# Kernel tuning notes

Hardware: AMD Instinct MI355X
Metric: run time of the kernel (lower is better)

## Reference

```python
import jax, jax.numpy as jnp
import numpy as np

B, N, D, E, F, K = 2, 2048, 768, 8, 3072, 2
V_MAX = 3.0
FEAT_CLAMP = 10.0


def setup_inputs() -> dict:
    key = jax.random.key(0)
    ks = jax.random.split(key, 8)
    s = lambda k, shape, sc: (jax.random.normal(k, shape, jnp.float32) * sc)
    return {
        "x": s(ks[0], (B, N, D), 1.0),
        "v_w": s(ks[1], (D,), 0.02),
        "v_b": jnp.zeros((), jnp.float32),
        "gate_w": s(ks[2], (D, E), 0.02),
        "gate_b": jnp.zeros((E,), jnp.float32),
        "w1": s(ks[3], (E, D, F), 0.02),
        "b1": jnp.zeros((E, F), jnp.float32),
        "w2": s(ks[4], (E, F, D), 0.02),
        "b2": jnp.zeros((E, D), jnp.float32),
        "out_w": s(ks[5], (2, D), 0.02),
        "out_b": jnp.zeros((D,), jnp.float32),
        "bk_scale": jnp.ones((D,), jnp.float32),
    }


def bk_green_diag(a):
    # a: (B, N) complex64 diagonal of (H_eps - z), unit off-diagonals.
    # Stable two-sided continued-fraction (Thomas/LDU) recursion:
    #   d_i = a_i - 1/d_{i-1},  e_i = a_i - 1/e_{i+1},  G_ii = 1/(d_i + e_i - a_i)
    aT = jnp.swapaxes(a, 0, 1)  # (N, B)

    def step(c, ai):
        d = ai - 1.0 / c
        return d, d

    d0 = aT[0]
    _, d_rest = jax.lax.scan(step, d0, aT[1:])
    d = jnp.concatenate([d0[None], d_rest], axis=0)  # (N, B)

    eN = aT[-1]
    _, e_rest = jax.lax.scan(step, eN, aT[:-1], reverse=True)
    e = jnp.concatenate([e_rest, eN[None]], axis=0)  # (N, B)

    G = 1.0 / (d + e - aT)
    return jnp.swapaxes(G, 0, 1)  # (B, N) complex


def reference(x, v_w, v_b, gate_w, gate_b, w1, b1, w2, b2, out_w, out_b, bk_scale):
    # --- potential projection: v = clamp(Linear(x), +-3) ---
    v = jnp.clip(x @ v_w + v_b, -V_MAX, V_MAX)  # (B, N)
    # H_eps diagonal = -2 + v, z = 1j  ->  A = H_eps - z
    a = ((-2.0 + v).astype(jnp.complex64) - 1j)
    G = bk_green_diag(a)  # (B, N) complex
    feats = jnp.stack([G.real, G.imag], axis=-1)  # (B, N, 2)

    # --- sparse MoE FFN (top-k softmax gating, GELU experts) ---
    logits = x @ gate_w + gate_b  # (B, N, E)
    probs = jax.nn.softmax(logits, axis=-1)
    topv, topi = jax.lax.top_k(probs, K)
    topv = topv / jnp.sum(topv, axis=-1, keepdims=True)
    comb = jnp.sum(topv[..., None] * jax.nn.one_hot(topi, E, dtype=x.dtype), axis=2)  # (B, N, E)
    h = jax.nn.gelu(jnp.einsum("bnd,edf->bnef", x, w1) + b1)  # (B, N, E, F)
    y = jnp.einsum("bnef,efd->bned", h, w2) + b2  # (B, N, E, D)
    ffn_out = jnp.einsum("bne,bned->bnd", comb, y)

    # --- spectral branch: clamp features, project to d_model, scale ---
    feats_c = jnp.clip(feats, -FEAT_CLAMP, FEAT_CLAMP)
    spec_out = feats_c @ out_w + out_b  # (B, N, D)
    return ffn_out + bk_scale * spec_out
```

## Files before the change

kernel.cpp:

```cpp
#include <hip/hip_runtime.h>
#include <hip/hip_bf16.h>

#define BB 2
#define NN 2048
#define DD 768
#define EE 8
#define FF 3072
#define TOK (BB*NN)
#define ROWS_CAP 9216
#define TILES 72

typedef __attribute__((ext_vector_type(8))) __bf16 bf16x8;
typedef __attribute__((ext_vector_type(4))) float floatx4;

#define OFF_CTRL    0ull
#define OFF_V       1024ull
#define OFF_TOKE    17408ull
#define OFF_TOKW    50176ull
#define OFF_ROWTOK  82944ull
#define OFF_ROWW    119808ull
#define OFF_SLOT    156672ull
#define OFF_FEATS   189440ull
#define OFF_W2T     222208ull
#define OFF_XBF     37970944ull
#define OFF_W1T     44262400ull
#define OFF_H       82011136ull
#define OFF_Y       OFF_XBF

__device__ __forceinline__ ushort f2b(float f) {
    union { float f; unsigned int i; } v; v.f = f;
    unsigned int u = v.i;
    unsigned int r = (u + 0x7FFFu + ((u >> 16) & 1u)) >> 16;
    return (ushort)r;
}
__device__ __forceinline__ unsigned int pk2(float lo, float hi) {
    union { float f; unsigned int u; } a, b;
    a.f = lo; b.f = hi;
    unsigned int ra = ((a.u + 0x7FFFu + ((a.u >> 16) & 1u)) >> 16) & 0xFFFFu;
    unsigned int rb = (b.u + 0x7FFFu + ((b.u >> 16) & 1u)) & 0xFFFF0000u;
    return ra | rb;
}
__device__ __forceinline__ float gelu_f(float x) {
    float z = 0.7978845608028654f * x * (1.f + 0.044715f * x * x);
    z = fminf(fmaxf(z, -12.f), 12.f);
    float e = __expf(2.f * z);
    return 0.5f * x * (1.f + (e - 1.f) / (e + 1.f));
}
__device__ __forceinline__ void gload16(const ushort* g, ushort* l) {
    __builtin_amdgcn_global_load_lds((const __attribute__((address_space(1))) void*)g,
                                     (__attribute__((address_space(3))) void*)l,
                                     16, 0, 0);
}

struct cplx { float x, y; };
__device__ __forceinline__ cplx cmulc(cplx a, cplx b) { return {a.x*b.x - a.y*b.y, a.x*b.y + a.y*b.x}; }
__device__ __forceinline__ cplx caddc(cplx a, cplx b) { return {a.x + b.x, a.y + b.y}; }
__device__ __forceinline__ cplx cdivc(cplx a, cplx b) {
    float s = 1.f / (b.x*b.x + b.y*b.y);
    return {(a.x*b.x + a.y*b.y)*s, (a.y*b.x - a.x*b.y)*s};
}
struct mob { cplx m00, m01, m10, m11; };
__device__ __forceinline__ mob mmul(const mob& A, const mob& B) {
    mob C;
    C.m00 = caddc(cmulc(A.m00, B.m00), cmulc(A.m01, B.m10));
    C.m01 = caddc(cmulc(A.m00, B.m01), cmulc(A.m01, B.m11));
    C.m10 = caddc(cmulc(A.m10, B.m00), cmulc(A.m11, B.m10));
    C.m11 = caddc(cmulc(A.m10, B.m01), cmulc(A.m11, B.m11));
    return C;
}
__device__ __forceinline__ void mnorm(mob& A) {
    float s = fabsf(A.m00.x);
    s = fmaxf(s, fabsf(A.m00.y)); s = fmaxf(s, fabsf(A.m01.x)); s = fmaxf(s, fabsf(A.m01.y));
    s = fmaxf(s, fabsf(A.m10.x)); s = fmaxf(s, fabsf(A.m10.y)); s = fmaxf(s, fabsf(A.m11.x));
    s = fmaxf(s, fabsf(A.m11.y));
    float r = 1.f / fmaxf(s, 1e-30f);
    A.m00.x *= r; A.m00.y *= r; A.m01.x *= r; A.m01.y *= r;
    A.m10.x *= r; A.m10.y *= r; A.m11.x *= r; A.m11.y *= r;
}
__device__ __forceinline__ mob mstep(cplx a, const mob& P) {
    mob C;
    C.m00 = {a.x*P.m00.x - a.y*P.m00.y - P.m10.x, a.x*P.m00.y + a.y*P.m00.x - P.m10.y};
    C.m01 = {a.x*P.m01.x - a.y*P.m01.y - P.m11.x, a.x*P.m01.y + a.y*P.m01.x - P.m11.y};
    C.m10 = P.m00; C.m11 = P.m01;
    return C;
}
__device__ __forceinline__ void mstore(float* s, const mob& A) {
    s[0]=A.m00.x; s[1]=A.m00.y; s[2]=A.m01.x; s[3]=A.m01.y;
    s[4]=A.m10.x; s[5]=A.m10.y; s[6]=A.m11.x; s[7]=A.m11.y;
}
__device__ __forceinline__ mob mload(const float* s) {
    mob A;
    A.m00 = {s[0], s[1]}; A.m01 = {s[2], s[3]};
    A.m10 = {s[4], s[5]}; A.m11 = {s[6], s[7]};
    return A;
}

template<bool PERM>
__device__ __forceinline__ void tcvt64_body(
    const float* __restrict__ src, ushort* __restrict__ dst,
    int Rs, int Cs, int r0, int c0, ushort* __restrict__ tT , int tid)
{
    int lr = tid >> 2;
    int lc0 = (tid & 3) * 16;
    const float* sp = src + (size_t)(r0 + lr) * Cs + c0 + lc0;
    float4 v[4];
    #pragma unroll
    for (int u = 0; u < 4; u++) v[u] = *(const float4*)(sp + 4*u);
    int chw = lr >> 3, wbit = lr & 7;
    #pragma unroll
    for (int u = 0; u < 4; u++) {
        float vs[4] = {v[u].x, v[u].y, v[u].z, v[u].w};
        #pragma unroll
        for (int e2 = 0; e2 < 4; e2++) {
            int col = lc0 + 4*u + e2;
            int g = (col >> 4) & 3;
            tT[col * 72 + ((chw ^ g) << 3) + wbit] = f2b(vs[e2]);
        }
    }
    __syncthreads();
    int p = tid & 7;
    #pragma unroll
    for (int pass = 0; pass < 2; pass++) {
        int c = (tid >> 3) + pass * 32;
        int g = (c >> 4) & 3;
        int chl = p ^ g;
        int a64 = chl * 8;
        size_t off = (size_t)(c0 + c) * Rs + r0 + a64;
        if (PERM) {
            int g32 = (a64 >> 5) * 32;
            int a = a64 & 31;
            ushort o8[8] __attribute__((aligned(16)));
            #pragma unroll
            for (int k = 0; k < 8; k++) {
                int pk = a + k;
                int rl = g32 + (pk >> 1) + ((pk & 1) << 4);
                int phys = ((rl >> 3) ^ g) * 8 + (rl & 7);
                o8[k] = tT[c * 72 + phys];
            }
            *(uint4*)(dst + off) = *(const uint4*)o8;
        } else {
            *(uint4*)(dst + off) = *(const uint4*)(tT + c * 72 + p * 8);
        }
    }
}

#define NB_CVT   ((TOK*DD)/8/256)
#define NB_ROUTE (TOK/4)

__device__ __forceinline__ void cvt_body(const float* __restrict__ src, ushort* __restrict__ dst, int i) {
    const float4* s = ((const float4*)src) + (size_t)i * 2;
    float4 a = s[0], b = s[1];
    uint4 o;
    o.x = pk2(a.x, a.y); o.y = pk2(a.z, a.w);
    o.z = pk2(b.x, b.y); o.w = pk2(b.z, b.w);
    *(((uint4*)dst) + i) = o;
}

__device__ __forceinline__ void routing_body(
    const float* __restrict__ x, const float* __restrict__ v_w, const float* __restrict__ v_b,
    const float* __restrict__ gate_w, const float* __restrict__ gate_b,
    float* __restrict__ v_out, int* __restrict__ tok_e, float* __restrict__ tok_w, int blk)
{
    int wave = threadIdx.x >> 6, lane = threadIdx.x & 63;
    int t = blk * 4 + wave;
    const float* xr = x + (size_t)t * DD;
    float av = 0.f;
    float ag[8] = {0.f, 0.f, 0.f, 0.f, 0.f, 0.f, 0.f, 0.f};
    #pragma unroll
    for (int i = 0; i < 12; i++) {
        int d = lane + 64 * i;
        float xv = xr[d];
        av += xv * v_w[d];
        const float4* g = (const float4*)(gate_w + d * 8);
        float4 g0 = g[0], g1 = g[1];
        ag[0] += xv * g0.x; ag[1] += xv * g0.y; ag[2] += xv * g0.z; ag[3] += xv * g0.w;
        ag[4] += xv * g1.x; ag[5] += xv * g1.y; ag[6] += xv * g1.z; ag[7] += xv * g1.w;
    }
    #pragma unroll
    for (int off = 32; off >= 1; off >>= 1) {
        av += __shfl_xor(av, off);
        #pragma unroll
        for (int e = 0; e < 8; e++) ag[e] += __shfl_xor(ag[e], off);
    }
    if (lane == 0) {
        float vv = av + v_b[0];
        vv = fminf(fmaxf(vv, -3.f), 3.f);
        v_out[t] = vv;
        float lg[8];
        #pragma unroll
        for (int e = 0; e < 8; e++) lg[e] = ag[e] + gate_b[e];
        int e0 = 0;
        #pragma unroll
        for (int e = 1; e < 8; e++) if (lg[e] > lg[e0]) e0 = e;
        int e1 = -1;
        #pragma unroll
        for (int e = 0; e < 8; e++) if (e != e0 && (e1 < 0 || lg[e] > lg[e1])) e1 = e;
        float w0 = 1.f / (1.f + __expf(lg[e1] - lg[e0]));
        tok_e[2*t] = e0; tok_e[2*t+1] = e1;
        tok_w[2*t] = w0; tok_w[2*t+1] = 1.f - w0;
    }
}

__global__ __launch_bounds__(256) void prep0_kernel(
    const float* __restrict__ x, ushort* __restrict__ x_bf,
    const float* __restrict__ v_w, const float* __restrict__ v_b,
    const float* __restrict__ gate_w, const float* __restrict__ gate_b,
    float* __restrict__ v_out, int* __restrict__ tok_e, float* __restrict__ tok_w)
{
    int id = blockIdx.x;
    if (id < NB_CVT) { cvt_body(x, x_bf, id * 256 + threadIdx.x); return; }
    id -= NB_CVT;
    routing_body(x, v_w, v_b, gate_w, gate_b, v_out, tok_e, tok_w, id);
}

#define NB_W1T4  (12*48*EE/4)

__device__ void setup_body(
    const int* __restrict__ tok_e, const float* __restrict__ tok_w,
    int* __restrict__ ctrl, int* __restrict__ row_token, float* __restrict__ row_w,
    int* __restrict__ slot)
{
    __shared__ int cnt[8], base[8], cursor[8];
    int tid = threadIdx.x;
    int lane = tid & 63;
    if (tid < 8) { cnt[tid] = 0; cursor[tid] = 0; }
    __syncthreads();

    int mye[8];
    #pragma unroll
    for (int it = 0; it < 8; it++) {
        int idx = it * 1024 + tid;
        int e = tok_e[idx];
        mye[it] = e;
        #pragma unroll
        for (int ex = 0; ex < 8; ex++) {
            unsigned long long m = __ballot(e == ex);
            if (e == ex && lane == (__ffsll((long long)m) - 1))
                atomicAdd(&cnt[ex], (int)__popcll(m));
        }
    }
    __syncthreads();
    if (tid == 0) {
        int b = 0;
        int* te = ctrl + 24;
        for (int i = 0; i < TILES; i++) te[i] = -1;
        #pragma unroll
        for (int e = 0; e < EE; e++) {
            base[e] = b;
            ctrl[16 + e] = b;
            int tiles = (cnt[e] + 127) >> 7;
            int t0 = b >> 7;
            for (int i = 0; i < tiles; i++) te[t0 + i] = e;
            b += tiles << 7;
        }
    }
    for (int p = tid; p < ROWS_CAP; p += 1024) row_token[p] = -1;
    __syncthreads();

    #pragma unroll
    for (int it = 0; it < 8; it++) {
        int idx = it * 1024 + tid;
        int e = mye[it];
        unsigned long long lt = (1ull << lane) - 1ull;
        int p = 0;
        #pragma unroll
        for (int ex = 0; ex < 8; ex++) {
            unsigned long long m = __ballot(e == ex);
            if (e == ex) {
                int leader = __ffsll((long long)m) - 1;
                int pos = (int)__popcll(m & lt);
                int bp = 0;
                if (lane == leader) bp = atomicAdd(&cursor[ex], (int)__popcll(m));
                bp = __shfl(bp, leader);
                p = base[ex] + bp + pos;
            }
        }
        row_token[p] = idx >> 1;
        row_w[p] = tok_w[idx];
        slot[idx] = p;
    }
}

__device__ void bk_body(int b, const float* __restrict__ v, float* __restrict__ feats) {
    int t = threadIdx.x;
    bool act = t < 256;
    __shared__ float sm[256][8];
    const mob I = {{1.f,0.f},{0.f,0.f},{0.f,0.f},{1.f,0.f}};
    cplx a[8];
    const float* vb = v + (size_t)b * NN;
    if (act) {
        #pragma unroll
        for (int j = 0; j < 8; j++) { a[j].x = -2.f + vb[t*8 + j]; a[j].y = -1.f; }
    }

    mob cur = I;
    if (act) {
        #pragma unroll
        for (int j = 0; j < 8; j++) cur = mstep(a[j], cur);
        mnorm(cur);
        mstore(sm[t], cur);
    }
    for (int s = 1; s < 256; s <<= 1) {
        __syncthreads();
        mob prev; bool has = act && (t >= s);
        if (has) prev = mload(sm[t - s]);
        __syncthreads();
        if (has) { cur = mmul(cur, prev); mnorm(cur); mstore(sm[t], cur); }
    }
    __syncthreads();
    cplx dreg[8];
    if (act) {
        mob P = (t > 0) ? mload(sm[t - 1]) : I;
        #pragma unroll
        for (int j = 0; j < 8; j++) {
            P = mstep(a[j], P); mnorm(P);
            dreg[j] = cdivc(P.m00, P.m10);
        }
    }
    __syncthreads();

    cur = I;
    if (act) {
        #pragma unroll
        for (int j = 7; j >= 0; j--) cur = mstep(a[j], cur);
        mnorm(cur);
        mstore(sm[t], cur);
    }
    for (int s = 1; s < 256; s <<= 1) {
        __syncthreads();
        mob nxt; bool has = act && (t + s < 256);
        if (has) nxt = mload(sm[t + s]);
        __syncthreads();
        if (has) { cur = mmul(cur, nxt); mnorm(cur); mstore(sm[t], cur); }
    }
    __syncthreads();
    if (act) {
        mob P = (t < 255) ? mload(sm[t + 1]) : I;
        #pragma unroll
        for (int j = 7; j >= 0; j--) {
            P = mstep(a[j], P); mnorm(P);
            cplx e = cdivc(P.m00, P.m10);
            cplx den = {dreg[j].x + e.x - a[j].x, dreg[j].y + e.y - a[j].y};
            cplx one = {1.f, 0.f};
            cplx G = cdivc(one, den);
            int i = b * NN + t*8 + j;
            feats[2*i]   = G.x;
            feats[2*i+1] = G.y;
        }
    }
}

__global__ __launch_bounds__(1024) void setup_bk_kernel(
    const int* __restrict__ tok_e, const float* __restrict__ tok_w,
    int* __restrict__ ctrl, int* __restrict__ row_token, float* __restrict__ row_w,
    int* __restrict__ slot, const float* __restrict__ v, float* __restrict__ feats,
    const float* __restrict__ w1, ushort* __restrict__ w1t)
{
    if (blockIdx.x == 0) { setup_body(tok_e, tok_w, ctrl, row_token, row_w, slot); return; }
    if (blockIdx.x <= BB) { bk_body(blockIdx.x - 1, v, feats); return; }
    __shared__ __align__(16) ushort tT4[4 * 4608];
    int tt = (blockIdx.x - 1 - BB) * 4 + (threadIdx.x >> 8);
    int e = tt / (12 * 48);
    int rem = tt - e * 12 * 48;
    int cy = rem / 12;
    int rx = rem - cy * 12;
    tcvt64_body<false>(w1 + (size_t)e * DD * FF, w1t + (size_t)e * FF * DD,
                       DD, FF, rx * 64, cy * 64,
                       tT4 + (threadIdx.x >> 8) * 4608, threadIdx.x & 255);
}

#define MFMAS() do { \
        _Pragma("unroll") \
        for (int i = 0; i < 4; i++) \
            _Pragma("unroll") \
            for (int j = 0; j < 4; j++) \
                acc[i][j] = __builtin_amdgcn_mfma_f32_16x16x32_bf16(afr[i], bfr[j], acc[i][j], 0, 0, 0); \
    } while (0)

#define G1N   (72 * 12)
#define NW2T  (48 * 12 * EE / 2)

__global__ __launch_bounds__(512, 2) void gemm1_fused_kernel(
    const ushort* __restrict__ x_bf, const ushort* __restrict__ w1t, const float* __restrict__ b1,
    const int* __restrict__ ctrl, const int* __restrict__ row_token, ushort* __restrict__ H,
    const float* __restrict__ w2, ushort* __restrict__ w2t)
{
    __shared__ __align__(16) ushort SH[73728];
    __shared__ int toks[128];
    int bid = blockIdx.x;
    int tid = threadIdx.x;

    if (bid >= G1N) {
        int tt = (bid - G1N) * 2 + (tid >> 8);
        int e = tt / (48 * 12);
        int rem = tt - e * 48 * 12;
        int cy = rem / 48;
        int rx = rem - cy * 48;
        ushort* tT = SH + (tid >> 8) * 4608;
        tcvt64_body<true>(w2 + (size_t)e * FF * DD, w2t + (size_t)e * DD * FF,
                          FF, DD, rx * 64, cy * 64, tT, tid & 255);
        return;
    }

    int x = bid & 7, s = bid >> 3;
    int fx = s / 9;
    int tile = x * 9 + (s - fx * 9);
    int e = ctrl[24 + tile];
    if (e < 0) return;
    int p0 = tile * 128;
    int f0 = fx * 256;

    ushort* B3 = SH + 3 * 8192;

    if (tid < 128) { int tk = row_token[p0 + tid]; toks[tid] = tk < 0 ? 0 : tk; }
    __syncthreads();

    int wave = tid >> 6, lane = tid & 63;
    int wr = wave >> 2, wc = wave & 3;
    int w16 = wave * 16;

    int srow = lane >> 3;
    int kq = ((lane & 7) ^ srow) * 8;
    int tokA0 = toks[w16 + srow];
    int tokA1 = toks[w16 + 8 + srow];
    const ushort* aA0 = x_bf + (size_t)tokA0 * DD + kq;
    const ushort* aA1 = x_bf + (size_t)tokA1 * DD + kq;
    const ushort* w1e = w1t + (size_t)e * (FF * DD);
    const ushort* bB00 = w1e + (size_t)(f0 +       w16 + srow) * DD + kq;
    const ushort* bB01 = w1e + (size_t)(f0 +       w16 + 8 + srow) * DD + kq;
    const ushort* bB10 = w1e + (size_t)(f0 + 128 + w16 + srow) * DD + kq;
    const ushort* bB11 = w1e + (size_t)(f0 + 128 + w16 + 8 + srow) * DD + kq;
    int dA0 = w16 * 64;
    int dA1 = dA0 + 512;

    int lm = lane & 15, q = lane >> 4;
    int qa0 = ((q    ) ^ (lm & 7)) * 8;
    int qa1 = ((q | 4) ^ (lm & 7)) * 8;
    int arow = (wr * 64 + lm) * 64;
    int brow = (wc * 64 + lm) * 64;

    floatx4 zero4 = {0.f, 0.f, 0.f, 0.f};
    floatx4 acc[4][4];
    #pragma unroll
    for (int i = 0; i < 4; i++)
        #pragma unroll
        for (int j = 0; j < 4; j++) acc[i][j] = zero4;

    #define STG_A(SL, kt) do { \
        gload16(aA0 + (kt)*64, SH + (SL)*8192 + dA0); \
        gload16(aA1 + (kt)*64, SH + (SL)*8192 + dA1); } while (0)
    #define STG_B(SL, kt) do { \
        gload16(bB00 + (kt)*64, B3 + (SL)*16384 + dA0); \
        gload16(bB01 + (kt)*64, B3 + (SL)*16384 + dA1); \
        gload16(bB10 + (kt)*64, B3 + (SL)*16384 + 8192 + dA0); \
        gload16(bB11 + (kt)*64, B3 + (SL)*16384 + 8192 + dA1); } while (0)

    #define G1_PHASE(SL, QH) do { \
        bf16x8 afr[4], bfr[4]; \
        _Pragma("unroll") \
        for (int i = 0; i < 4; i++) \
            afr[i] = *(const bf16x8*)(const void*)(SH + (SL)*8192 + arow + i*1024 + (QH)); \
        _Pragma("unroll") \
        for (int j = 0; j < 4; j++) \
            bfr[j] = *(const bf16x8*)(const void*)(B3 + (SL)*16384 + brow + j*1024 + (QH)); \
        asm volatile("s_waitcnt lgkmcnt(0)" ::: "memory"); \
        __builtin_amdgcn_sched_barrier(0); \
        __builtin_amdgcn_s_setprio(1); \
        MFMAS(); \
        __builtin_amdgcn_s_setprio(0); } while (0)

    #define G1_TILE(kt, SL, S2) do { \
        bool st_ = (kt) < 10; \
        if (st_) STG_A(S2, (kt) + 2); \
        G1_PHASE(SL, qa0); \
        __builtin_amdgcn_s_barrier(); \
        if (st_) STG_B(S2, (kt) + 2); \
        G1_PHASE(SL, qa1); \
        if (st_)            { asm volatile("s_waitcnt vmcnt(6)" ::: "memory"); } \
        else if ((kt) < 11) { asm volatile("s_waitcnt vmcnt(0)" ::: "memory"); } \
        __builtin_amdgcn_s_barrier(); } while (0)

    STG_A(0, 0); STG_B(0, 0);
    STG_A(1, 1); STG_B(1, 1);
    asm volatile("s_waitcnt vmcnt(6)" ::: "memory");
    __builtin_amdgcn_s_barrier();

    for (int kb = 0; kb < 12; kb += 3) {
        G1_TILE(kb    , 0, 2);
        G1_TILE(kb + 1, 1, 0);
        G1_TILE(kb + 2, 2, 1);
    }
    #undef G1_TILE
    #undef G1_PHASE
    #undef STG_B
    #undef STG_A

    #pragma unroll
    for (int i = 0; i < 4; i++) {
        #pragma unroll
        for (int jp = 0; jp < 2; jp++) {
            float bias0 = b1[e * FF + f0 + wc*64 + (2*jp)*16 + lm];
            float bias1 = b1[e * FF + f0 + wc*64 + (2*jp+1)*16 + lm];
            #pragma unroll
            for (int r = 0; r < 4; r++) {
                int m = wr*64 + i*16 + q*4 + r;
                float h0 = gelu_f(acc[i][2*jp][r] + bias0);
                float h1 = gelu_f(acc[i][2*jp+1][r] + bias1);
                *(unsigned int*)(H + (size_t)(p0 + m) * FF + f0 + wc*64 + jp*32 + lm*2) = pk2(h0, h1);
            }
        }
    }
}

#define STAGE64(AW, BW, k0) do { \
        _Pragma("unroll") \
        for (int g = 0; g < 4; g++) { \
            gload16(ag[g] + (k0), (AW) + g*8*64); \
            gload16(bg[g] + (k0), (BW) + g*8*64); \
        } } while (0)

#define LOADFR64(APTR, BPTR, QX) do { \
        _Pragma("unroll") \
        for (int i = 0; i < 4; i++) \
            afr[i] = *(const bf16x8*)(const void*)((APTR) + (wm + i*16 + lm) * 64 + (QX)); \
        _Pragma("unroll") \
        for (int j = 0; j < 4; j++) \
            bfr[j] = *(const bf16x8*)(const void*)((BPTR) + (wn + j*16 + lm) * 64 + (QX)); \
    } while (0)

#define PIPE64(NK) do { \
    STAGE64(AsW0, BsW0, 0); \
    STAGE64(AsW1, BsW1, 64); \
    for (int ks = 0; ks < (NK); ks++) { \
        int cur = ks & 1; \
        const ushort* Ab = cur ? As[1] : As[0]; \
        const ushort* Bb = cur ? Bs[1] : Bs[0]; \
        ushort* AsN = cur ? AsW1 : AsW0; \
        ushort* BsN = cur ? BsW1 : BsW0; \
        if (ks < (NK) - 1) { asm volatile("s_waitcnt vmcnt(8)" ::: "memory"); } \
        else               { asm volatile("s_waitcnt vmcnt(0)" ::: "memory"); } \
        __builtin_amdgcn_s_barrier(); \
        { \
            bf16x8 afr[4], bfr[4]; \
            LOADFR64(Ab, Bb, qx0); \
            __builtin_amdgcn_s_setprio(1); \
            MFMAS(); \
            __builtin_amdgcn_s_setprio(0); \
        } \
        { \
            bf16x8 afr[4], bfr[4]; \
            LOADFR64(Ab, Bb, qx0 ^ 32); \
            asm volatile("s_waitcnt lgkmcnt(0)" ::: "memory"); \
            __builtin_amdgcn_sched_barrier(0); \
            __builtin_amdgcn_s_barrier(); \
            if (ks + 2 < (NK)) STAGE64(AsN, BsN, ks*64 + 128); \
            __builtin_amdgcn_s_setprio(1); \
            MFMAS(); \
            __builtin_amdgcn_s_setprio(0); \
        } \
    } } while (0)

__global__ __launch_bounds__(256) void gemm2_kernel(
    const ushort* __restrict__ H, const ushort* __restrict__ w2t, const float* __restrict__ b2,
    const int* __restrict__ ctrl, const float* __restrict__ row_w, float* __restrict__ Y)
{
    int tile = blockIdx.x;
    int e = ctrl[24 + tile];
    if (e < 0) return;
    int p0 = tile * 128;
    int d0 = blockIdx.y * 128;

    __shared__ ushort As[2][128 * 64];
    __shared__ ushort Bs[2][128 * 64];

    int tid = threadIdx.x;
    int wave = tid >> 6, lane = tid & 63;
    int srow = lane >> 3;
    int kq = (((lane & 7) ^ (srow & 7))) * 8;
    const ushort* ag[4];
    #pragma unroll
    for (int g = 0; g < 4; g++)
        ag[g] = H + (size_t)(p0 + wave*32 + g*8 + srow) * FF + kq;
    const ushort* w2e = w2t + (size_t)e * (DD * FF);
    const ushort* bg[4];
    #pragma unroll
    for (int g = 0; g < 4; g++)
        bg[g] = w2e + (size_t)(d0 + wave*32 + g*8 + srow) * FF + kq;
    ushort* AsW0 = &As[0][wave * 32 * 64];
    ushort* BsW0 = &Bs[0][wave * 32 * 64];
    ushort* AsW1 = &As[1][wave * 32 * 64];
    ushort* BsW1 = &Bs[1][wave * 32 * 64];

    floatx4 zero4 = {0.f, 0.f, 0.f, 0.f};
    floatx4 acc[4][4];
    #pragma unroll
    for (int i = 0; i < 4; i++)
        #pragma unroll
        for (int j = 0; j < 4; j++) acc[i][j] = zero4;

    int wm = (wave & 1) * 64, wn = (wave >> 1) * 64;
    int lm = lane & 15, q = lane >> 4;
    int qx0 = (q ^ (lm & 7)) * 8;

    PIPE64(FF/64);

    #pragma unroll
    for (int i = 0; i < 4; i++) {
        #pragma unroll
        for (int j = 0; j < 4; j++) {
            int n = wn + j*16 + lm;
            float bias = b2[e * DD + d0 + n];
            #pragma unroll
            for (int r = 0; r < 4; r++) {
                int m = wm + i*16 + q*4 + r;
                float wgt = row_w[p0 + m];
                Y[(size_t)(p0 + m) * DD + d0 + n] = wgt * (acc[i][j][r] + bias);
            }
        }
    }
}

__global__ __launch_bounds__(256) void final_kernel(
    const float* __restrict__ Y, const int* __restrict__ slot, const float* __restrict__ feats,
    const float* __restrict__ out_w, const float* __restrict__ out_b,
    const float* __restrict__ bk_scale, float* __restrict__ out)
{
    int idx = blockIdx.x * 256 + threadIdx.x;
    int base = idx * 4;
    int t = base / DD;
    int d = base - t * DD;
    int p0 = slot[2*t], p1 = slot[2*t + 1];
    const float4 ya = *(const float4*)(Y + (size_t)p0 * DD + d);
    const float4 yb = *(const float4*)(Y + (size_t)p1 * DD + d);
    float f0 = feats[2*t], f1 = feats[2*t + 1];
    f0 = fminf(fmaxf(f0, -10.f), 10.f);
    f1 = fminf(fmaxf(f1, -10.f), 10.f);
    float ff[4] = {ya.x + yb.x, ya.y + yb.y, ya.z + yb.z, ya.w + yb.w};
    float4 o;
    float* op = (float*)&o;
    #pragma unroll
    for (int u = 0; u < 4; u++) {
        float spec = f0 * out_w[d + u] + f1 * out_w[DD + d + u] + out_b[d + u];
        op[u] = ff[u] + bk_scale[d + u] * spec;
    }
    *(float4*)(out + base) = o;
}

extern "C" void kernel_launch(void* const* d_in, const int* in_sizes, int n_in,
                              void* d_out, int out_size, void* d_ws, size_t ws_size,
                              hipStream_t stream)
{
    const float* x      = (const float*)d_in[0];
    const float* v_w    = (const float*)d_in[1];
    const float* v_b    = (const float*)d_in[2];
    const float* gate_w = (const float*)d_in[3];
    const float* gate_b = (const float*)d_in[4];
    const float* w1     = (const float*)d_in[5];
    const float* b1     = (const float*)d_in[6];
    const float* w2     = (const float*)d_in[7];
    const float* b2     = (const float*)d_in[8];
    const float* out_w  = (const float*)d_in[9];
    const float* out_b  = (const float*)d_in[10];
    const float* bk_s   = (const float*)d_in[11];

    char* ws = (char*)d_ws;
    int*    ctrl    = (int*)(ws + OFF_CTRL);
    float*  v       = (float*)(ws + OFF_V);
    int*    tok_e   = (int*)(ws + OFF_TOKE);
    float*  tok_w   = (float*)(ws + OFF_TOKW);
    int*    row_tok = (int*)(ws + OFF_ROWTOK);
    float*  row_w   = (float*)(ws + OFF_ROWW);
    int*    slot    = (int*)(ws + OFF_SLOT);
    float*  feats   = (float*)(ws + OFF_FEATS);
    ushort* w2t     = (ushort*)(ws + OFF_W2T);
    ushort* x_bf    = (ushort*)(ws + OFF_XBF);
    ushort* w1t     = (ushort*)(ws + OFF_W1T);
    ushort* H       = (ushort*)(ws + OFF_H);
    float*  Y       = (float*)(ws + OFF_Y);
    float*  out     = (float*)d_out;

    prep0_kernel<<<NB_CVT + NB_ROUTE, 256, 0, stream>>>(
        x, x_bf, v_w, v_b, gate_w, gate_b, v, tok_e, tok_w);
    setup_bk_kernel<<<1 + BB + NB_W1T4, 1024, 0, stream>>>(
        tok_e, tok_w, ctrl, row_tok, row_w, slot, v, feats, w1, w1t);
    gemm1_fused_kernel<<<G1N + NW2T, 512, 0, stream>>>(x_bf, w1t, b1, ctrl, row_tok, H, w2, w2t);
    gemm2_kernel<<<dim3(TILES, DD / 128), 256, 0, stream>>>(H, w2t, b2, ctrl, row_w, Y);
    final_kernel<<<(TOK * DD) / 1024, 256, 0, stream>>>(Y, slot, feats, out_w, out_b, bk_s, out);
}
```

Measured before the change: 208.1 us.

## Halve gemm1 K-tile to 32 to shrink LDS and raise occupancy

Reduces the gemm1 K step from 64 to 32, which halves the triple-buffered LDS footprint (SH from 147KB to 74KB). Launch bounds change from 2 to 4 blocks per CU, and the load/swizzle mapping, per-phase fragment reads and vmcnt/barrier schedule are rewritten for 24 single-phase iterations. The aim is more resident blocks to hide global latency, at the cost of twice as many barriers and a tighter register budget that may force spills.

```diff
diff --git a/kernel.cpp b/kernel.cpp
--- a/kernel.cpp
+++ b/kernel.cpp
@@ -380,12 +380,12 @@
 #define G1N   (72 * 12)
 #define NW2T  (48 * 12 * EE / 2)
 
-__global__ __launch_bounds__(512, 2) void gemm1_fused_kernel(
+__global__ __launch_bounds__(512, 4) void gemm1_fused_kernel(
     const ushort* __restrict__ x_bf, const ushort* __restrict__ w1t, const float* __restrict__ b1,
     const int* __restrict__ ctrl, const int* __restrict__ row_token, ushort* __restrict__ H,
     const float* __restrict__ w2, ushort* __restrict__ w2t)
 {
-    __shared__ __align__(16) ushort SH[73728];
+    __shared__ __align__(16) ushort SH[36864];
     __shared__ int toks[128];
     int bid = blockIdx.x;
     int tid = threadIdx.x;
@@ -410,34 +410,28 @@
     int p0 = tile * 128;
     int f0 = fx * 256;
 
-    ushort* B3 = SH + 3 * 8192;
+    ushort* Bb = SH + 3 * 4096;
 
     if (tid < 128) { int tk = row_token[p0 + tid]; toks[tid] = tk < 0 ? 0 : tk; }
     __syncthreads();
 
     int wave = tid >> 6, lane = tid & 63;
     int wr = wave >> 2, wc = wave & 3;
-    int w16 = wave * 16;
-
-    int srow = lane >> 3;
-    int kq = ((lane & 7) ^ srow) * 8;
-    int tokA0 = toks[w16 + srow];
-    int tokA1 = toks[w16 + 8 + srow];
-    const ushort* aA0 = x_bf + (size_t)tokA0 * DD + kq;
-    const ushort* aA1 = x_bf + (size_t)tokA1 * DD + kq;
+
+    int rsub = lane >> 2;
+    int kq = (((lane & 3) ^ ((rsub >> 1) & 3))) * 8;
+    int tokA = toks[wave * 16 + rsub];
+    const ushort* aglob = x_bf + (size_t)tokA * DD + kq;
     const ushort* w1e = w1t + (size_t)e * (FF * DD);
-    const ushort* bB00 = w1e + (size_t)(f0 +       w16 + srow) * DD + kq;
-    const ushort* bB01 = w1e + (size_t)(f0 +       w16 + 8 + srow) * DD + kq;
-    const ushort* bB10 = w1e + (size_t)(f0 + 128 + w16 + srow) * DD + kq;
-    const ushort* bB11 = w1e + (size_t)(f0 + 128 + w16 + 8 + srow) * DD + kq;
-    int dA0 = w16 * 64;
-    int dA1 = dA0 + 512;
+    const ushort* bglob0 = w1e + (size_t)(f0 + wave * 32 + rsub) * DD + kq;
+    const ushort* bglob1 = bglob0 + (size_t)16 * DD;
+    int dA  = wave * 512;
+    int dB0 = wave * 1024, dB1 = dB0 + 512;
 
     int lm = lane & 15, q = lane >> 4;
-    int qa0 = ((q    ) ^ (lm & 7)) * 8;
-    int qa1 = ((q | 4) ^ (lm & 7)) * 8;
-    int arow = (wr * 64 + lm) * 64;
-    int brow = (wc * 64 + lm) * 64;
+    int qx = (q ^ ((lm >> 1) & 3)) * 8;
+    int arow = (wr * 64 + lm) * 32;
+    int brow = (wc * 64 + lm) * 32;
 
     floatx4 zero4 = {0.f, 0.f, 0.f, 0.f};
     floatx4 acc[4][4];
@@ -446,54 +440,41 @@
         #pragma unroll
         for (int j = 0; j < 4; j++) acc[i][j] = zero4;
 
-    #define STG_A(SL, kt) do { \
-        gload16(aA0 + (kt)*64, SH + (SL)*8192 + dA0); \
-        gload16(aA1 + (kt)*64, SH + (SL)*8192 + dA1); } while (0)
-    #define STG_B(SL, kt) do { \
-        gload16(bB00 + (kt)*64, B3 + (SL)*16384 + dA0); \
-        gload16(bB01 + (kt)*64, B3 + (SL)*16384 + dA1); \
-        gload16(bB10 + (kt)*64, B3 + (SL)*16384 + 8192 + dA0); \
-        gload16(bB11 + (kt)*64, B3 + (SL)*16384 + 8192 + dA1); } while (0)
-
-    #define G1_PHASE(SL, QH) do { \
+    #define STG(SL, kt) do { \
+        gload16(aglob  + (kt)*32, SH + (SL)*4096 + dA); \
+        gload16(bglob0 + (kt)*32, Bb + (SL)*8192 + dB0); \
+        gload16(bglob1 + (kt)*32, Bb + (SL)*8192 + dB1); } while (0)
+
+    #define TILE1(kt, SL, S2) do { \
+        bool st_ = (kt) < 22; \
+        if (st_) STG(S2, (kt) + 2); \
         bf16x8 afr[4], bfr[4]; \
         _Pragma("unroll") \
         for (int i = 0; i < 4; i++) \
-            afr[i] = *(const bf16x8*)(const void*)(SH + (SL)*8192 + arow + i*1024 + (QH)); \
+            afr[i] = *(const bf16x8*)(const void*)(SH + (SL)*4096 + arow + i*512 + qx); \
         _Pragma("unroll") \
         for (int j = 0; j < 4; j++) \
-            bfr[j] = *(const bf16x8*)(const void*)(B3 + (SL)*16384 + brow + j*1024 + (QH)); \
+            bfr[j] = *(const bf16x8*)(const void*)(Bb + (SL)*8192 + brow + j*512 + qx); \
         asm volatile("s_waitcnt lgkmcnt(0)" ::: "memory"); \
         __builtin_amdgcn_sched_barrier(0); \
         __builtin_amdgcn_s_setprio(1); \
         MFMAS(); \
-        __builtin_amdgcn_s_setprio(0); } while (0)
-
-    #define G1_TILE(kt, SL, S2) do { \
-        bool st_ = (kt) < 10; \
-        if (st_) STG_A(S2, (kt) + 2); \
-        G1_PHASE(SL, qa0); \
-        __builtin_amdgcn_s_barrier(); \
-        if (st_) STG_B(S2, (kt) + 2); \
-        G1_PHASE(SL, qa1); \
-        if (st_)            { asm volatile("s_waitcnt vmcnt(6)" ::: "memory"); } \
-        else if ((kt) < 11) { asm volatile("s_waitcnt vmcnt(0)" ::: "memory"); } \
-        __builtin_amdgcn_s_barrier(); } while (0)
-
-    STG_A(0, 0); STG_B(0, 0);
-    STG_A(1, 1); STG_B(1, 1);
-    asm volatile("s_waitcnt vmcnt(6)" ::: "memory");
+        __builtin_amdgcn_s_setprio(0); \
+        if (st_)             { asm volatile("s_waitcnt vmcnt(3)" ::: "memory"); } \
+        else if ((kt) == 22) { asm volatile("s_waitcnt vmcnt(0)" ::: "memory"); } \
+        if ((kt) < 23) __builtin_amdgcn_s_barrier(); } while (0)
+
+    STG(0, 0); STG(1, 1);
+    asm volatile("s_waitcnt vmcnt(3)" ::: "memory");
     __builtin_amdgcn_s_barrier();
 
-    for (int kb = 0; kb < 12; kb += 3) {
-        G1_TILE(kb    , 0, 2);
-        G1_TILE(kb + 1, 1, 0);
-        G1_TILE(kb + 2, 2, 1);
-    }
-    #undef G1_TILE
-    #undef G1_PHASE
-    #undef STG_B
-    #undef STG_A
+    for (int kb = 0; kb < 24; kb += 3) {
+        TILE1(kb    , 0, 2);
+        TILE1(kb + 1, 1, 0);
+        TILE1(kb + 2, 2, 1);
+    }
+    #undef TILE1
+    #undef STG
 
     #pragma unroll
     for (int i = 0; i < 4; i++) {
```

Result: faster. 183.5 us (median of 2 runs) (-11.8%).
